# Kernel tuning notes

Measured on AMD Instinct MI355X. Metric: run time of the kernel, lower is better.

The kernel has to match this reference:

```python
import jax, jax.numpy as jnp
import numpy as np

B = 16384
IN = 512
H = 512

def setup_inputs() -> dict:
    key = jax.random.key(0)
    ks = jax.random.split(key, 8)
    inp = {
        "x_t": jax.random.normal(ks[0], (B, IN), dtype=jnp.float32),
        "h_t": jax.random.normal(ks[1], (B, H), dtype=jnp.float32),
        "W_ir": jax.random.normal(ks[2], (IN, H), dtype=jnp.float32),
        "W_hr": jax.random.normal(ks[3], (H, H), dtype=jnp.float32),
        "b_r": jnp.zeros((H,), dtype=jnp.float32),
        "W_iz": jax.random.normal(ks[4], (IN, H), dtype=jnp.float32),
        "W_hz": jax.random.normal(ks[5], (H, H), dtype=jnp.float32),
        "b_z": jnp.zeros((H,), dtype=jnp.float32),
        "W_in": jax.random.normal(ks[6], (IN, H), dtype=jnp.float32),
        "W_hn": jax.random.normal(ks[7], (H, H), dtype=jnp.float32),
        "b_n": jnp.zeros((H,), dtype=jnp.float32),
    }
    return inp

def reference(x_t, h_t, W_ir, W_hr, b_r, W_iz, W_hz, b_z, W_in, W_hn, b_n):
    # Fuse the three input-side and three hidden-side GEMMs by concatenating weights.
    Wi = jnp.concatenate([W_ir, W_iz, W_in], axis=1)   # [IN, 3H]
    Wh = jnp.concatenate([W_hr, W_hz, W_hn], axis=1)   # [H, 3H]
    gi = x_t @ Wi                                      # [B, 3H]
    gh = h_t @ Wh                                      # [B, 3H]
    h = b_r.shape[0]
    r_t = jax.nn.sigmoid(gi[:, :h] + gh[:, :h] + b_r)
    z_t = jax.nn.sigmoid(gi[:, h:2*h] + gh[:, h:2*h] + b_z)
    n_t = jnp.tanh(gi[:, 2*h:] + r_t * gh[:, 2*h:] + b_n)
    return (1.0 - z_t) * n_t + z_t * h_t
```

## Files before the change

kernel.cpp:

```cpp
#include <hip/hip_runtime.h>
#include <hip/hip_fp16.h>

typedef _Float16 half8 __attribute__((ext_vector_type(8)));
typedef float floatx4 __attribute__((ext_vector_type(4)));

#define AS1 __attribute__((address_space(1)))
#define AS3 __attribute__((address_space(3)))

#define WLO_OFF (6 * 512 * 512)

__device__ __forceinline__ void async_lds16(const void* g, void* l) {
  __builtin_amdgcn_global_load_lds((const AS1 void*)g, (AS3 void*)l, 16, 0, 0);
}

__global__ __launch_bounds__(256) void permute_w(
    const float* __restrict__ Wir, const float* __restrict__ Whr,
    const float* __restrict__ Wiz, const float* __restrict__ Whz,
    const float* __restrict__ Win, const float* __restrict__ Whn,
    _Float16* __restrict__ wperm) {
  __shared__ __align__(16) float tile[32 * 68];
  const int b = blockIdx.x;
  const int w = b >> 7;
  const int rem = b & 127;
  const int ki = rem >> 3;
  const int nt = rem & 7;
  const float* W = (w == 0) ? Wir : (w == 1) ? Whr : (w == 2) ? Wiz
                 : (w == 3) ? Whz : (w == 4) ? Win : Whn;
  const int k0 = ki * 32, n0 = nt * 64;
  const int t = threadIdx.x;

  const int kk = t >> 3;
  const int nn = (t & 7) * 8;
  const float* src = W + (k0 + kk) * 512 + n0 + nn;
  float4 f0 = *(const float4*)(src);
  float4 f1 = *(const float4*)(src + 4);
  float* drow = tile + kk * 68 + nn;
  *(float4*)(drow) = f0;
  *(float4*)(drow + 4) = f1;
  __syncthreads();

  const int u = t >> 6, l = t & 63;
  const int nloc = 16 * u + (l & 15);
  const int kbase = 8 * (l >> 4);
  half8 vh, vl;
#pragma unroll
  for (int j = 0; j < 8; ++j) {
    float f = tile[(kbase + j) * 68 + nloc];
    _Float16 hi = (_Float16)f;
    _Float16 lo = (_Float16)(f - (float)hi);
    vh[j] = hi;
    vl[j] = lo;
  }
  const size_t off = ((size_t)((w * 8 + nt) * 16 + ki)) * 2048 + t * 8;
  *(half8*)(wperm + off) = vh;
  *(half8*)(wperm + WLO_OFF + off) = vl;
}

__global__ __launch_bounds__(256, 2) void gru_fused(
    const float* __restrict__ x, const float* __restrict__ h,
    const _Float16* __restrict__ wperm,
    const float* __restrict__ br, const float* __restrict__ bz,
    const float* __restrict__ bn, float* __restrict__ out) {
  __shared__ __align__(16) _Float16 ldsXh[128 * 32];
  __shared__ __align__(16) _Float16 ldsXl[128 * 32];
  __shared__ __align__(16) _Float16 ldsHh[128 * 32];
  __shared__ __align__(16) _Float16 ldsHl[128 * 32];
  __shared__ __align__(16) _Float16 ldsW[6 * 2048];

  const int t = threadIdx.x;
  const int lane = t & 63;
  const int wv = t >> 6;
  const int wm = wv >> 1;
  const int wn = wv & 1;
  const int bid = blockIdx.x;
  const int nt = bid & 7;
  const int mt = bid >> 3;
  const int m0 = mt * 128;
  const int n0 = nt * 64;
  const _Float16* wlo = wperm + WLO_OFF;

  floatx4 acc_r[4][2] = {};
  floatx4 acc_z[4][2] = {};
  floatx4 acc_in[4][2] = {};
  floatx4 acc_hn[4][2] = {};

  const int c0 = t, c1 = t + 256;
  const int s0 = c0 >> 6, l0 = c0 & 63;
  const int s1 = c1 >> 6, l1 = c1 & 63;
  const int mA0 = 16 * s0 + (l0 & 15), kA0 = 8 * (l0 >> 4);
  const int mA1 = 16 * s1 + (l1 & 15), kA1 = 8 * (l1 >> 4);

  for (int kt = 0; kt < 16; ++kt) {
    const int k0 = kt * 32;
    __syncthreads();

#pragma unroll
    for (int q = 0; q < 6; ++q) {
      const int gg = wv * 6 + q;
      const int w = gg >> 2, u = gg & 3;
      const char* gsrc = (const char*)wperm +
          ((size_t)((w * 8 + nt) * 16 + kt)) * 4096 + u * 1024 + lane * 16;
      char* ldst = (char*)ldsW + (w * 4 + u) * 1024;
      async_lds16(gsrc, ldst);
    }

    {
      const float* px0 = x + (m0 + mA0) * 512 + k0 + kA0;
      const float* px1 = x + (m0 + mA1) * 512 + k0 + kA1;
      const float* ph0 = h + (m0 + mA0) * 512 + k0 + kA0;
      const float* ph1 = h + (m0 + mA1) * 512 + k0 + kA1;
      float v[4][8];
      *(float4*)&v[0][0] = *(const float4*)px0; *(float4*)&v[0][4] = *(const float4*)(px0 + 4);
      *(float4*)&v[1][0] = *(const float4*)px1; *(float4*)&v[1][4] = *(const float4*)(px1 + 4);
      *(float4*)&v[2][0] = *(const float4*)ph0; *(float4*)&v[2][4] = *(const float4*)(ph0 + 4);
      *(float4*)&v[3][0] = *(const float4*)ph1; *(float4*)&v[3][4] = *(const float4*)(ph1 + 4);
      half8 hi[4], lo[4];
#pragma unroll
      for (int g = 0; g < 4; ++g) {
#pragma unroll
        for (int j = 0; j < 8; ++j) {
          _Float16 a = (_Float16)v[g][j];
          hi[g][j] = a;
          lo[g][j] = (_Float16)(v[g][j] - (float)a);
        }
      }
      *(half8*)(ldsXh + c0 * 8) = hi[0]; *(half8*)(ldsXl + c0 * 8) = lo[0];
      *(half8*)(ldsXh + c1 * 8) = hi[1]; *(half8*)(ldsXl + c1 * 8) = lo[1];
      *(half8*)(ldsHh + c0 * 8) = hi[2]; *(half8*)(ldsHl + c0 * 8) = lo[2];
      *(half8*)(ldsHh + c1 * 8) = hi[3]; *(half8*)(ldsHl + c1 * 8) = lo[3];
    }
    __syncthreads();

    half8 axh[4], ahh[4];
#pragma unroll
    for (int i = 0; i < 4; ++i) {
      axh[i] = *(const half8*)(ldsXh + ((wm * 4 + i) * 64 + lane) * 8);
      ahh[i] = *(const half8*)(ldsHh + ((wm * 4 + i) * 64 + lane) * 8);
    }
#pragma unroll
    for (int jn = 0; jn < 2; ++jn) {
      const int bo = (wn * 2 + jn) * 512 + lane * 8;
      const size_t tb = ((size_t)(nt * 16 + kt)) * 2048 + bo;
      half8 bl_ir = *(const half8*)(wlo + tb + (size_t)0 * 8 * 16 * 2048);
      half8 bl_hr = *(const half8*)(wlo + tb + (size_t)1 * 8 * 16 * 2048);
      half8 bl_iz = *(const half8*)(wlo + tb + (size_t)2 * 8 * 16 * 2048);
      half8 bl_hz = *(const half8*)(wlo + tb + (size_t)3 * 8 * 16 * 2048);
      half8 bl_in = *(const half8*)(wlo + tb + (size_t)4 * 8 * 16 * 2048);
      half8 bl_hn = *(const half8*)(wlo + tb + (size_t)5 * 8 * 16 * 2048);
      half8 bh_ir = *(const half8*)(ldsW + 0 * 2048 + bo);
      half8 bh_hr = *(const half8*)(ldsW + 1 * 2048 + bo);
      half8 bh_iz = *(const half8*)(ldsW + 2 * 2048 + bo);
      half8 bh_hz = *(const half8*)(ldsW + 3 * 2048 + bo);
      half8 bh_in = *(const half8*)(ldsW + 4 * 2048 + bo);
      half8 bh_hn = *(const half8*)(ldsW + 5 * 2048 + bo);
#pragma unroll
      for (int i = 0; i < 4; ++i) {
        half8 axl = *(const half8*)(ldsXl + ((wm * 4 + i) * 64 + lane) * 8);
        half8 ahl = *(const half8*)(ldsHl + ((wm * 4 + i) * 64 + lane) * 8);
        acc_r[i][jn]  = __builtin_amdgcn_mfma_f32_16x16x32_f16(axh[i], bh_ir, acc_r[i][jn], 0, 0, 0);
        acc_r[i][jn]  = __builtin_amdgcn_mfma_f32_16x16x32_f16(axl,    bh_ir, acc_r[i][jn], 0, 0, 0);
        acc_r[i][jn]  = __builtin_amdgcn_mfma_f32_16x16x32_f16(ahh[i], bh_hr, acc_r[i][jn], 0, 0, 0);
        acc_r[i][jn]  = __builtin_amdgcn_mfma_f32_16x16x32_f16(ahl,    bh_hr, acc_r[i][jn], 0, 0, 0);
        acc_z[i][jn]  = __builtin_amdgcn_mfma_f32_16x16x32_f16(axh[i], bh_iz, acc_z[i][jn], 0, 0, 0);
        acc_z[i][jn]  = __builtin_amdgcn_mfma_f32_16x16x32_f16(axl,    bh_iz, acc_z[i][jn], 0, 0, 0);
        acc_z[i][jn]  = __builtin_amdgcn_mfma_f32_16x16x32_f16(ahh[i], bh_hz, acc_z[i][jn], 0, 0, 0);
        acc_z[i][jn]  = __builtin_amdgcn_mfma_f32_16x16x32_f16(ahl,    bh_hz, acc_z[i][jn], 0, 0, 0);
        acc_in[i][jn] = __builtin_amdgcn_mfma_f32_16x16x32_f16(axh[i], bh_in, acc_in[i][jn], 0, 0, 0);
        acc_in[i][jn] = __builtin_amdgcn_mfma_f32_16x16x32_f16(axl,    bh_in, acc_in[i][jn], 0, 0, 0);
        acc_hn[i][jn] = __builtin_amdgcn_mfma_f32_16x16x32_f16(ahh[i], bh_hn, acc_hn[i][jn], 0, 0, 0);
        acc_hn[i][jn] = __builtin_amdgcn_mfma_f32_16x16x32_f16(ahl,    bh_hn, acc_hn[i][jn], 0, 0, 0);
      }
#pragma unroll
      for (int i = 0; i < 4; ++i) {
        acc_r[i][jn]  = __builtin_amdgcn_mfma_f32_16x16x32_f16(axh[i], bl_ir, acc_r[i][jn], 0, 0, 0);
        acc_r[i][jn]  = __builtin_amdgcn_mfma_f32_16x16x32_f16(ahh[i], bl_hr, acc_r[i][jn], 0, 0, 0);
        acc_z[i][jn]  = __builtin_amdgcn_mfma_f32_16x16x32_f16(axh[i], bl_iz, acc_z[i][jn], 0, 0, 0);
        acc_z[i][jn]  = __builtin_amdgcn_mfma_f32_16x16x32_f16(ahh[i], bl_hz, acc_z[i][jn], 0, 0, 0);
        acc_in[i][jn] = __builtin_amdgcn_mfma_f32_16x16x32_f16(axh[i], bl_in, acc_in[i][jn], 0, 0, 0);
        acc_hn[i][jn] = __builtin_amdgcn_mfma_f32_16x16x32_f16(ahh[i], bl_hn, acc_hn[i][jn], 0, 0, 0);
      }
    }
  }

  const int quad = lane >> 4;
  const int col = lane & 15;
#pragma unroll
  for (int i = 0; i < 4; ++i) {
    const int mbase = m0 + wm * 64 + i * 16 + quad * 4;
#pragma unroll
    for (int jn = 0; jn < 2; ++jn) {
      const int n = n0 + wn * 32 + jn * 16 + col;
      const float vbr = br[n], vbz = bz[n], vbn = bn[n];
#pragma unroll
      for (int r = 0; r < 4; ++r) {
        const int m = mbase + r;
        const float gr = acc_r[i][jn][r] + vbr;
        const float gz = acc_z[i][jn][r] + vbz;
        const float rg = 1.0f / (1.0f + __expf(-gr));
        const float zg = 1.0f / (1.0f + __expf(-gz));
        const float gn = acc_in[i][jn][r] + rg * acc_hn[i][jn][r] + vbn;
        const float e2 = __expf(2.0f * gn);
        const float ntv = 1.0f - 2.0f / (e2 + 1.0f);
        const float hp = h[m * 512 + n];
        out[m * 512 + n] = (1.0f - zg) * ntv + zg * hp;
      }
    }
  }
}

extern "C" void kernel_launch(void* const* d_in, const int* in_sizes, int n_in,
                              void* d_out, int out_size, void* d_ws, size_t ws_size,
                              hipStream_t stream) {
  const float* x   = (const float*)d_in[0];
  const float* h   = (const float*)d_in[1];
  const float* Wir = (const float*)d_in[2];
  const float* Whr = (const float*)d_in[3];
  const float* br  = (const float*)d_in[4];
  const float* Wiz = (const float*)d_in[5];
  const float* Whz = (const float*)d_in[6];
  const float* bz  = (const float*)d_in[7];
  const float* Win = (const float*)d_in[8];
  const float* Whn = (const float*)d_in[9];
  const float* bn  = (const float*)d_in[10];
  float* out = (float*)d_out;
  _Float16* wperm = (_Float16*)d_ws;

  permute_w<<<768, 256, 0, stream>>>(Wir, Whr, Wiz, Whz, Win, Whn, wperm);
  gru_fused<<<1024, 256, 0, stream>>>(x, h, wperm, br, bz, bn, out);
}
```

Before: 282.2 us.

## Pre-split x/h into fp16 hi/lo tiles and stream them via async LDS loads

A preprocessing pass now converts x and h once into pre-tiled fp16 hi/lo buffers in the workspace. The main kernel then copies those tiles straight into LDS with global_load_lds, instead of loading fp32 and converting in registers on every block. Without this, each of the 8 N-tile blocks sharing an M-tile repeats the conversion. The change also adds an XCD-aware block swizzle so the blocks sharing an M-tile land on the same XCD. The cost is a large extra write and read of the converted activations through memory, and it needs a big workspace; if the workspace is too small, the code falls back to the old conversion path.

```diff
diff --git a/kernel.cpp b/kernel.cpp
--- a/kernel.cpp
+++ b/kernel.cpp
@@ -7,19 +7,55 @@
 #define AS1 __attribute__((address_space(1)))
 #define AS3 __attribute__((address_space(3)))
 
-#define WLO_OFF (6 * 512 * 512)
+#define WLO_OFF   (6 * 512 * 512)
+#define XH_BASE   (2 * WLO_OFF)
+#define XH_LO_OFF (2 * 16384 * 512)
+#define WS_NEED   ((size_t)(XH_BASE + 2 * XH_LO_OFF) * 2)
 
 __device__ __forceinline__ void async_lds16(const void* g, void* l) {
   __builtin_amdgcn_global_load_lds((const AS1 void*)g, (AS3 void*)l, 16, 0, 0);
 }
 
-__global__ __launch_bounds__(256) void permute_w(
+__global__ __launch_bounds__(256) void preprocess(
+    const float* __restrict__ x, const float* __restrict__ h,
     const float* __restrict__ Wir, const float* __restrict__ Whr,
     const float* __restrict__ Wiz, const float* __restrict__ Whz,
     const float* __restrict__ Win, const float* __restrict__ Whn,
-    _Float16* __restrict__ wperm) {
+    _Float16* __restrict__ ws, int do_xh) {
+  const int t = threadIdx.x;
+  const int bid = blockIdx.x;
+  if (do_xh && bid < 4096) {
+    const int mat = bid >> 11;
+    const int rem = bid & 2047;
+    const int mt = rem >> 4, kt = rem & 15;
+    const float* src = mat ? h : x;
+    const size_t tb = (size_t)(mat * 2048 + mt * 16 + kt) * 4096;
+    _Float16* hi = ws + XH_BASE;
+    _Float16* lo = hi + XH_LO_OFF;
+#pragma unroll
+    for (int cc = 0; cc < 2; ++cc) {
+      const int c = t + cc * 256;
+      const int l = c & 63, s = c >> 6;
+      const int m = mt * 128 + 16 * s + (l & 15);
+      const int k = kt * 32 + 8 * (l >> 4);
+      const float* p = src + (size_t)m * 512 + k;
+      float4 f0 = *(const float4*)p;
+      float4 f1 = *(const float4*)(p + 4);
+      float v[8] = {f0.x, f0.y, f0.z, f0.w, f1.x, f1.y, f1.z, f1.w};
+      half8 vh, vl;
+#pragma unroll
+      for (int j = 0; j < 8; ++j) {
+        _Float16 a = (_Float16)v[j];
+        vh[j] = a;
+        vl[j] = (_Float16)(v[j] - (float)a);
+      }
+      *(half8*)(hi + tb + c * 8) = vh;
+      *(half8*)(lo + tb + c * 8) = vl;
+    }
+    return;
+  }
+  const int b = do_xh ? (bid - 4096) : bid;
   __shared__ __align__(16) float tile[32 * 68];
-  const int b = blockIdx.x;
   const int w = b >> 7;
   const int rem = b & 127;
   const int ki = rem >> 3;
@@ -27,8 +63,6 @@
   const float* W = (w == 0) ? Wir : (w == 1) ? Whr : (w == 2) ? Wiz
                  : (w == 3) ? Whz : (w == 4) ? Win : Whn;
   const int k0 = ki * 32, n0 = nt * 64;
-  const int t = threadIdx.x;
-
   const int kk = t >> 3;
   const int nn = (t & 7) * 8;
   const float* src = W + (k0 + kk) * 512 + n0 + nn;
@@ -38,7 +72,6 @@
   *(float4*)(drow) = f0;
   *(float4*)(drow + 4) = f1;
   __syncthreads();
-
   const int u = t >> 6, l = t & 63;
   const int nloc = 16 * u + (l & 15);
   const int kbase = 8 * (l >> 4);
@@ -46,25 +79,30 @@
 #pragma unroll
   for (int j = 0; j < 8; ++j) {
     float f = tile[(kbase + j) * 68 + nloc];
-    _Float16 hi = (_Float16)f;
-    _Float16 lo = (_Float16)(f - (float)hi);
-    vh[j] = hi;
-    vl[j] = lo;
+    _Float16 hiv = (_Float16)f;
+    vh[j] = hiv;
+    vl[j] = (_Float16)(f - (float)hiv);
   }
   const size_t off = ((size_t)((w * 8 + nt) * 16 + ki)) * 2048 + t * 8;
-  *(half8*)(wperm + off) = vh;
-  *(half8*)(wperm + WLO_OFF + off) = vl;
-}
-
-__global__ __launch_bounds__(256, 2) void gru_fused(
-    const float* __restrict__ x, const float* __restrict__ h,
-    const _Float16* __restrict__ wperm,
+  *(half8*)(ws + off) = vh;
+  *(half8*)(ws + WLO_OFF + off) = vl;
+}
+
+__device__ __forceinline__ void swizzle_mn(int bid, int& mt, int& nt) {
+  const int xcd = bid & 7;
+  const int u = bid >> 3;
+  nt = u & 7;
+  mt = ((u >> 3) << 3) | xcd;
+}
+
+__global__ __launch_bounds__(256, 2) void gru_dma(
+    const float* __restrict__ h, const _Float16* __restrict__ ws,
     const float* __restrict__ br, const float* __restrict__ bz,
     const float* __restrict__ bn, float* __restrict__ out) {
-  __shared__ __align__(16) _Float16 ldsXh[128 * 32];
-  __shared__ __align__(16) _Float16 ldsXl[128 * 32];
-  __shared__ __align__(16) _Float16 ldsHh[128 * 32];
-  __shared__ __align__(16) _Float16 ldsHl[128 * 32];
+  __shared__ __align__(16) _Float16 ldsXh[4096];
+  __shared__ __align__(16) _Float16 ldsXl[4096];
+  __shared__ __align__(16) _Float16 ldsHh[4096];
+  __shared__ __align__(16) _Float16 ldsHl[4096];
   __shared__ __align__(16) _Float16 ldsW[6 * 2048];
 
   const int t = threadIdx.x;
@@ -72,62 +110,47 @@
   const int wv = t >> 6;
   const int wm = wv >> 1;
   const int wn = wv & 1;
-  const int bid = blockIdx.x;
-  const int nt = bid & 7;
-  const int mt = bid >> 3;
+  int mt, nt;
+  swizzle_mn(blockIdx.x, mt, nt);
   const int m0 = mt * 128;
   const int n0 = nt * 64;
-  const _Float16* wlo = wperm + WLO_OFF;
+
+  const _Float16* whi = ws;
+  const _Float16* wlo = ws + WLO_OFF;
+  const _Float16* xhhi = ws + XH_BASE;
+  const _Float16* xhlo = xhhi + XH_LO_OFF;
 
   floatx4 acc_r[4][2] = {};
   floatx4 acc_z[4][2] = {};
   floatx4 acc_in[4][2] = {};
   floatx4 acc_hn[4][2] = {};
 
-  const int c0 = t, c1 = t + 256;
-  const int s0 = c0 >> 6, l0 = c0 & 63;
-  const int s1 = c1 >> 6, l1 = c1 & 63;
-  const int mA0 = 16 * s0 + (l0 & 15), kA0 = 8 * (l0 >> 4);
-  const int mA1 = 16 * s1 + (l1 & 15), kA1 = 8 * (l1 >> 4);
-
   for (int kt = 0; kt < 16; ++kt) {
-    const int k0 = kt * 32;
     __syncthreads();
 
 #pragma unroll
-    for (int q = 0; q < 6; ++q) {
-      const int gg = wv * 6 + q;
-      const int w = gg >> 2, u = gg & 3;
-      const char* gsrc = (const char*)wperm +
-          ((size_t)((w * 8 + nt) * 16 + kt)) * 4096 + u * 1024 + lane * 16;
-      char* ldst = (char*)ldsW + (w * 4 + u) * 1024;
+    for (int q = 0; q < 14; ++q) {
+      const int g = wv * 14 + q;
+      const char* gsrc;
+      char* ldst;
+      if (g < 24) {
+        const int w = g >> 2, uu = g & 3;
+        gsrc = (const char*)whi + ((size_t)((w * 8 + nt) * 16 + kt)) * 4096 +
+               uu * 1024 + (size_t)lane * 16;
+        ldst = (char*)ldsW + (w * 4 + uu) * 1024;
+      } else {
+        const int g2 = g - 24;
+        const int buf = g2 >> 3, seg = g2 & 7;
+        const int mat = buf >> 1;
+        const int part = buf & 1;
+        const _Float16* base = part ? xhlo : xhhi;
+        gsrc = (const char*)base + ((size_t)(mat * 2048 + mt * 16 + kt)) * 8192 +
+               seg * 1024 + (size_t)lane * 16;
+        _Float16* lb = (buf == 0) ? ldsXh : (buf == 1) ? ldsXl
+                     : (buf == 2) ? ldsHh : ldsHl;
+        ldst = (char*)lb + seg * 1024;
+      }
       async_lds16(gsrc, ldst);
-    }
-
-    {
-      const float* px0 = x + (m0 + mA0) * 512 + k0 + kA0;
-      const float* px1 = x + (m0 + mA1) * 512 + k0 + kA1;
-      const float* ph0 = h + (m0 + mA0) * 512 + k0 + kA0;
-      const float* ph1 = h + (m0 + mA1) * 512 + k0 + kA1;
-      float v[4][8];
-      *(float4*)&v[0][0] = *(const float4*)px0; *(float4*)&v[0][4] = *(const float4*)(px0 + 4);
-      *(float4*)&v[1][0] = *(const float4*)px1; *(float4*)&v[1][4] = *(const float4*)(px1 + 4);
-      *(float4*)&v[2][0] = *(const float4*)ph0; *(float4*)&v[2][4] = *(const float4*)(ph0 + 4);
-      *(float4*)&v[3][0] = *(const float4*)ph1; *(float4*)&v[3][4] = *(const float4*)(ph1 + 4);
-      half8 hi[4], lo[4];
-#pragma unroll
-      for (int g = 0; g < 4; ++g) {
-#pragma unroll
-        for (int j = 0; j < 8; ++j) {
-          _Float16 a = (_Float16)v[g][j];
-          hi[g][j] = a;
-          lo[g][j] = (_Float16)(v[g][j] - (float)a);
-        }
-      }
-      *(half8*)(ldsXh + c0 * 8) = hi[0]; *(half8*)(ldsXl + c0 * 8) = lo[0];
-      *(half8*)(ldsXh + c1 * 8) = hi[1]; *(half8*)(ldsXl + c1 * 8) = lo[1];
-      *(half8*)(ldsHh + c0 * 8) = hi[2]; *(half8*)(ldsHl + c0 * 8) = lo[2];
-      *(half8*)(ldsHh + c1 * 8) = hi[3]; *(half8*)(ldsHl + c1 * 8) = lo[3];
     }
     __syncthreads();
 
@@ -208,6 +231,155 @@
   }
 }
 
+__global__ __launch_bounds__(256, 2) void gru_conv(
+    const float* __restrict__ x, const float* __restrict__ h,
+    const _Float16* __restrict__ wperm,
+    const float* __restrict__ br, const float* __restrict__ bz,
+    const float* __restrict__ bn, float* __restrict__ out) {
+  __shared__ __align__(16) _Float16 ldsXh[128 * 32];
+  __shared__ __align__(16) _Float16 ldsXl[128 * 32];
+  __shared__ __align__(16) _Float16 ldsHh[128 * 32];
+  __shared__ __align__(16) _Float16 ldsHl[128 * 32];
+  __shared__ __align__(16) _Float16 ldsW[6 * 2048];
+
+  const int t = threadIdx.x;
+  const int lane = t & 63;
+  const int wv = t >> 6;
+  const int wm = wv >> 1;
+  const int wn = wv & 1;
+  int mt, nt;
+  swizzle_mn(blockIdx.x, mt, nt);
+  const int m0 = mt * 128;
+  const int n0 = nt * 64;
+  const _Float16* wlo = wperm + WLO_OFF;
+
+  floatx4 acc_r[4][2] = {};
+  floatx4 acc_z[4][2] = {};
+  floatx4 acc_in[4][2] = {};
+  floatx4 acc_hn[4][2] = {};
+
+  const int c0 = t, c1 = t + 256;
+  const int s0 = c0 >> 6, l0 = c0 & 63;
+  const int s1 = c1 >> 6, l1 = c1 & 63;
+  const int mA0 = 16 * s0 + (l0 & 15), kA0 = 8 * (l0 >> 4);
+  const int mA1 = 16 * s1 + (l1 & 15), kA1 = 8 * (l1 >> 4);
+
+  for (int kt = 0; kt < 16; ++kt) {
+    const int k0 = kt * 32;
+    __syncthreads();
+#pragma unroll
+    for (int q = 0; q < 6; ++q) {
+      const int gg = wv * 6 + q;
+      const int w = gg >> 2, u = gg & 3;
+      const char* gsrc = (const char*)wperm +
+          ((size_t)((w * 8 + nt) * 16 + kt)) * 4096 + u * 1024 + lane * 16;
+      char* ldst = (char*)ldsW + (w * 4 + u) * 1024;
+      async_lds16(gsrc, ldst);
+    }
+    {
+      const float* px0 = x + (m0 + mA0) * 512 + k0 + kA0;
+      const float* px1 = x + (m0 + mA1) * 512 + k0 + kA1;
+      const float* ph0 = h + (m0 + mA0) * 512 + k0 + kA0;
+      const float* ph1 = h + (m0 + mA1) * 512 + k0 + kA1;
+      float v[4][8];
+      *(float4*)&v[0][0] = *(const float4*)px0; *(float4*)&v[0][4] = *(const float4*)(px0 + 4);
+      *(float4*)&v[1][0] = *(const float4*)px1; *(float4*)&v[1][4] = *(const float4*)(px1 + 4);
+      *(float4*)&v[2][0] = *(const float4*)ph0; *(float4*)&v[2][4] = *(const float4*)(ph0 + 4);
+      *(float4*)&v[3][0] = *(const float4*)ph1; *(float4*)&v[3][4] = *(const float4*)(ph1 + 4);
+      half8 hi[4], lo[4];
+#pragma unroll
+      for (int g = 0; g < 4; ++g) {
+#pragma unroll
+        for (int j = 0; j < 8; ++j) {
+          _Float16 a = (_Float16)v[g][j];
+          hi[g][j] = a;
+          lo[g][j] = (_Float16)(v[g][j] - (float)a);
+        }
+      }
+      *(half8*)(ldsXh + c0 * 8) = hi[0]; *(half8*)(ldsXl + c0 * 8) = lo[0];
+      *(half8*)(ldsXh + c1 * 8) = hi[1]; *(half8*)(ldsXl + c1 * 8) = lo[1];
+      *(half8*)(ldsHh + c0 * 8) = hi[2]; *(half8*)(ldsHl + c0 * 8) = lo[2];
+      *(half8*)(ldsHh + c1 * 8) = hi[3]; *(half8*)(ldsHl + c1 * 8) = lo[3];
+    }
+    __syncthreads();
+
+    half8 axh[4], ahh[4];
+#pragma unroll
+    for (int i = 0; i < 4; ++i) {
+      axh[i] = *(const half8*)(ldsXh + ((wm * 4 + i) * 64 + lane) * 8);
+      ahh[i] = *(const half8*)(ldsHh + ((wm * 4 + i) * 64 + lane) * 8);
+    }
+#pragma unroll
+    for (int jn = 0; jn < 2; ++jn) {
+      const int bo = (wn * 2 + jn) * 512 + lane * 8;
+      const size_t tb = ((size_t)(nt * 16 + kt)) * 2048 + bo;
+      half8 bl_ir = *(const half8*)(wlo + tb + (size_t)0 * 8 * 16 * 2048);
+      half8 bl_hr = *(const half8*)(wlo + tb + (size_t)1 * 8 * 16 * 2048);
+      half8 bl_iz = *(const half8*)(wlo + tb + (size_t)2 * 8 * 16 * 2048);
+      half8 bl_hz = *(const half8*)(wlo + tb + (size_t)3 * 8 * 16 * 2048);
+      half8 bl_in = *(const half8*)(wlo + tb + (size_t)4 * 8 * 16 * 2048);
+      half8 bl_hn = *(const half8*)(wlo + tb + (size_t)5 * 8 * 16 * 2048);
+      half8 bh_ir = *(const half8*)(ldsW + 0 * 2048 + bo);
+      half8 bh_hr = *(const half8*)(ldsW + 1 * 2048 + bo);
+      half8 bh_iz = *(const half8*)(ldsW + 2 * 2048 + bo);
+      half8 bh_hz = *(const half8*)(ldsW + 3 * 2048 + bo);
+      half8 bh_in = *(const half8*)(ldsW + 4 * 2048 + bo);
+      half8 bh_hn = *(const half8*)(ldsW + 5 * 2048 + bo);
+#pragma unroll
+      for (int i = 0; i < 4; ++i) {
+        half8 axl = *(const half8*)(ldsXl + ((wm * 4 + i) * 64 + lane) * 8);
+        half8 ahl = *(const half8*)(ldsHl + ((wm * 4 + i) * 64 + lane) * 8);
+        acc_r[i][jn]  = __builtin_amdgcn_mfma_f32_16x16x32_f16(axh[i], bh_ir, acc_r[i][jn], 0, 0, 0);
+        acc_r[i][jn]  = __builtin_amdgcn_mfma_f32_16x16x32_f16(axl,    bh_ir, acc_r[i][jn], 0, 0, 0);
+        acc_r[i][jn]  = __builtin_amdgcn_mfma_f32_16x16x32_f16(ahh[i], bh_hr, acc_r[i][jn], 0, 0, 0);
+        acc_r[i][jn]  = __builtin_amdgcn_mfma_f32_16x16x32_f16(ahl,    bh_hr, acc_r[i][jn], 0, 0, 0);
+        acc_z[i][jn]  = __builtin_amdgcn_mfma_f32_16x16x32_f16(axh[i], bh_iz, acc_z[i][jn], 0, 0, 0);
+        acc_z[i][jn]  = __builtin_amdgcn_mfma_f32_16x16x32_f16(axl,    bh_iz, acc_z[i][jn], 0, 0, 0);
+        acc_z[i][jn]  = __builtin_amdgcn_mfma_f32_16x16x32_f16(ahh[i], bh_hz, acc_z[i][jn], 0, 0, 0);
+        acc_z[i][jn]  = __builtin_amdgcn_mfma_f32_16x16x32_f16(ahl,    bh_hz, acc_z[i][jn], 0, 0, 0);
+        acc_in[i][jn] = __builtin_amdgcn_mfma_f32_16x16x32_f16(axh[i], bh_in, acc_in[i][jn], 0, 0, 0);
+        acc_in[i][jn] = __builtin_amdgcn_mfma_f32_16x16x32_f16(axl,    bh_in, acc_in[i][jn], 0, 0, 0);
+        acc_hn[i][jn] = __builtin_amdgcn_mfma_f32_16x16x32_f16(ahh[i], bh_hn, acc_hn[i][jn], 0, 0, 0);
+        acc_hn[i][jn] = __builtin_amdgcn_mfma_f32_16x16x32_f16(ahl,    bh_hn, acc_hn[i][jn], 0, 0, 0);
+      }
+#pragma unroll
+      for (int i = 0; i < 4; ++i) {
+        acc_r[i][jn]  = __builtin_amdgcn_mfma_f32_16x16x32_f16(axh[i], bl_ir, acc_r[i][jn], 0, 0, 0);
+        acc_r[i][jn]  = __builtin_amdgcn_mfma_f32_16x16x32_f16(ahh[i], bl_hr, acc_r[i][jn], 0, 0, 0);
+        acc_z[i][jn]  = __builtin_amdgcn_mfma_f32_16x16x32_f16(axh[i], bl_iz, acc_z[i][jn], 0, 0, 0);
+        acc_z[i][jn]  = __builtin_amdgcn_mfma_f32_16x16x32_f16(ahh[i], bl_hz, acc_z[i][jn], 0, 0, 0);
+        acc_in[i][jn] = __builtin_amdgcn_mfma_f32_16x16x32_f16(axh[i], bl_in, acc_in[i][jn], 0, 0, 0);
+        acc_hn[i][jn] = __builtin_amdgcn_mfma_f32_16x16x32_f16(ahh[i], bl_hn, acc_hn[i][jn], 0, 0, 0);
+      }
+    }
+  }
+
+  const int quad = lane >> 4;
+  const int col = lane & 15;
+#pragma unroll
+  for (int i = 0; i < 4; ++i) {
+    const int mbase = m0 + wm * 64 + i * 16 + quad * 4;
+#pragma unroll
+    for (int jn = 0; jn < 2; ++jn) {
+      const int n = n0 + wn * 32 + jn * 16 + col;
+      const float vbr = br[n], vbz = bz[n], vbn = bn[n];
+#pragma unroll
+      for (int r = 0; r < 4; ++r) {
+        const int m = mbase + r;
+        const float gr = acc_r[i][jn][r] + vbr;
+        const float gz = acc_z[i][jn][r] + vbz;
+        const float rg = 1.0f / (1.0f + __expf(-gr));
+        const float zg = 1.0f / (1.0f + __expf(-gz));
+        const float gn = acc_in[i][jn][r] + rg * acc_hn[i][jn][r] + vbn;
+        const float e2 = __expf(2.0f * gn);
+        const float ntv = 1.0f - 2.0f / (e2 + 1.0f);
+        const float hp = h[m * 512 + n];
+        out[m * 512 + n] = (1.0f - zg) * ntv + zg * hp;
+      }
+    }
+  }
+}
+
 extern "C" void kernel_launch(void* const* d_in, const int* in_sizes, int n_in,
                               void* d_out, int out_size, void* d_ws, size_t ws_size,
                               hipStream_t stream) {
@@ -223,8 +395,13 @@
   const float* Whn = (const float*)d_in[9];
   const float* bn  = (const float*)d_in[10];
   float* out = (float*)d_out;
-  _Float16* wperm = (_Float16*)d_ws;
-
-  permute_w<<<768, 256, 0, stream>>>(Wir, Whr, Wiz, Whz, Win, Whn, wperm);
-  gru_fused<<<1024, 256, 0, stream>>>(x, h, wperm, br, bz, bn, out);
-}
+  _Float16* ws = (_Float16*)d_ws;
+
+  if (ws_size >= WS_NEED) {
+    preprocess<<<4096 + 768, 256, 0, stream>>>(x, h, Wir, Whr, Wiz, Whz, Win, Whn, ws, 1);
+    gru_dma<<<1024, 256, 0, stream>>>(h, ws, br, bz, bn, out);
+  } else {
+    preprocess<<<768, 256, 0, stream>>>(x, h, Wir, Whr, Wiz, Whz, Win, Whn, ws, 0);
+    gru_conv<<<1024, 256, 0, stream>>>(x, h, ws, br, bz, bn, out);
+  }
+}
```

Measured after the change: 500.7 us. +77.4%, slower.

## Prefetch next x/h tile into registers and read hi weights directly from global

Applied to the files above, without the earlier changes.

Register-prefetches the next K-slice of x and h during the MFMA loop and converts it to hi/lo fp16 after the compute, so global load latency overlaps with math. It also drops the async global-to-LDS staging of the high-part weights and loads them straight from global/L2 into registers, as the low parts already were. This cuts LDS usage and a sync dependency but adds register pressure and more uncoalesced-free global weight reads per wave. The final iteration prefetches a wrapped slice that is never used.

```diff
diff --git a/kernel.cpp b/kernel.cpp
--- a/kernel.cpp
+++ b/kernel.cpp
@@ -4,14 +4,8 @@
 typedef _Float16 half8 __attribute__((ext_vector_type(8)));
 typedef float floatx4 __attribute__((ext_vector_type(4)));
 
-#define AS1 __attribute__((address_space(1)))
-#define AS3 __attribute__((address_space(3)))
-
 #define WLO_OFF (6 * 512 * 512)
-
-__device__ __forceinline__ void async_lds16(const void* g, void* l) {
-  __builtin_amdgcn_global_load_lds((const AS1 void*)g, (AS3 void*)l, 16, 0, 0);
-}
+#define WSTRIDE ((size_t)(8 * 16 * 2048))
 
 __global__ __launch_bounds__(256) void permute_w(
     const float* __restrict__ Wir, const float* __restrict__ Whr,
@@ -46,14 +40,24 @@
 #pragma unroll
   for (int j = 0; j < 8; ++j) {
     float f = tile[(kbase + j) * 68 + nloc];
-    _Float16 hi = (_Float16)f;
-    _Float16 lo = (_Float16)(f - (float)hi);
-    vh[j] = hi;
-    vl[j] = lo;
+    _Float16 hiv = (_Float16)f;
+    vh[j] = hiv;
+    vl[j] = (_Float16)(f - (float)hiv);
   }
   const size_t off = ((size_t)((w * 8 + nt) * 16 + ki)) * 2048 + t * 8;
   *(half8*)(wperm + off) = vh;
   *(half8*)(wperm + WLO_OFF + off) = vl;
+}
+
+__device__ __forceinline__ void cvt_hilo(const float4 a, const float4 b,
+                                         half8& hi, half8& lo) {
+  const float v[8] = {a.x, a.y, a.z, a.w, b.x, b.y, b.z, b.w};
+#pragma unroll
+  for (int j = 0; j < 8; ++j) {
+    _Float16 hv = (_Float16)v[j];
+    hi[j] = hv;
+    lo[j] = (_Float16)(v[j] - (float)hv);
+  }
 }
 
 __global__ __launch_bounds__(256, 2) void gru_fused(
@@ -61,11 +65,10 @@
     const _Float16* __restrict__ wperm,
     const float* __restrict__ br, const float* __restrict__ bz,
     const float* __restrict__ bn, float* __restrict__ out) {
-  __shared__ __align__(16) _Float16 ldsXh[128 * 32];
-  __shared__ __align__(16) _Float16 ldsXl[128 * 32];
-  __shared__ __align__(16) _Float16 ldsHh[128 * 32];
-  __shared__ __align__(16) _Float16 ldsHl[128 * 32];
-  __shared__ __align__(16) _Float16 ldsW[6 * 2048];
+  __shared__ __align__(16) _Float16 ldsXh[4096];
+  __shared__ __align__(16) _Float16 ldsXl[4096];
+  __shared__ __align__(16) _Float16 ldsHh[4096];
+  __shared__ __align__(16) _Float16 ldsHl[4096];
 
   const int t = threadIdx.x;
   const int lane = t & 63;
@@ -77,6 +80,7 @@
   const int mt = bid >> 3;
   const int m0 = mt * 128;
   const int n0 = nt * 64;
+  const _Float16* whi = wperm;
   const _Float16* wlo = wperm + WLO_OFF;
 
   floatx4 acc_r[4][2] = {};
@@ -85,51 +89,41 @@
   floatx4 acc_hn[4][2] = {};
 
   const int c0 = t, c1 = t + 256;
-  const int s0 = c0 >> 6, l0 = c0 & 63;
-  const int s1 = c1 >> 6, l1 = c1 & 63;
-  const int mA0 = 16 * s0 + (l0 & 15), kA0 = 8 * (l0 >> 4);
-  const int mA1 = 16 * s1 + (l1 & 15), kA1 = 8 * (l1 >> 4);
+  const int l0 = c0 & 63, l1 = c1 & 63;
+  const int mA0 = 16 * (c0 >> 6) + (l0 & 15), kA0 = 8 * (l0 >> 4);
+  const int mA1 = 16 * (c1 >> 6) + (l1 & 15), kA1 = 8 * (l1 >> 4);
+  const float* pxb0 = x + (size_t)(m0 + mA0) * 512 + kA0;
+  const float* pxb1 = x + (size_t)(m0 + mA1) * 512 + kA1;
+  const float* phb0 = h + (size_t)(m0 + mA0) * 512 + kA0;
+  const float* phb1 = h + (size_t)(m0 + mA1) * 512 + kA1;
+
+  half8 sth[4], stl[4];
+  cvt_hilo(*(const float4*)pxb0, *(const float4*)(pxb0 + 4), sth[0], stl[0]);
+  cvt_hilo(*(const float4*)pxb1, *(const float4*)(pxb1 + 4), sth[1], stl[1]);
+  cvt_hilo(*(const float4*)phb0, *(const float4*)(phb0 + 4), sth[2], stl[2]);
+  cvt_hilo(*(const float4*)phb1, *(const float4*)(phb1 + 4), sth[3], stl[3]);
 
   for (int kt = 0; kt < 16; ++kt) {
-    const int k0 = kt * 32;
     __syncthreads();
-
-#pragma unroll
-    for (int q = 0; q < 6; ++q) {
-      const int gg = wv * 6 + q;
-      const int w = gg >> 2, u = gg & 3;
-      const char* gsrc = (const char*)wperm +
-          ((size_t)((w * 8 + nt) * 16 + kt)) * 4096 + u * 1024 + lane * 16;
-      char* ldst = (char*)ldsW + (w * 4 + u) * 1024;
-      async_lds16(gsrc, ldst);
-    }
-
-    {
-      const float* px0 = x + (m0 + mA0) * 512 + k0 + kA0;
-      const float* px1 = x + (m0 + mA1) * 512 + k0 + kA1;
-      const float* ph0 = h + (m0 + mA0) * 512 + k0 + kA0;
-      const float* ph1 = h + (m0 + mA1) * 512 + k0 + kA1;
-      float v[4][8];
-      *(float4*)&v[0][0] = *(const float4*)px0; *(float4*)&v[0][4] = *(const float4*)(px0 + 4);
-      *(float4*)&v[1][0] = *(const float4*)px1; *(float4*)&v[1][4] = *(const float4*)(px1 + 4);
-      *(float4*)&v[2][0] = *(const float4*)ph0; *(float4*)&v[2][4] = *(const float4*)(ph0 + 4);
-      *(float4*)&v[3][0] = *(const float4*)ph1; *(float4*)&v[3][4] = *(const float4*)(ph1 + 4);
-      half8 hi[4], lo[4];
-#pragma unroll
-      for (int g = 0; g < 4; ++g) {
-#pragma unroll
-        for (int j = 0; j < 8; ++j) {
-          _Float16 a = (_Float16)v[g][j];
-          hi[g][j] = a;
-          lo[g][j] = (_Float16)(v[g][j] - (float)a);
-        }
-      }
-      *(half8*)(ldsXh + c0 * 8) = hi[0]; *(half8*)(ldsXl + c0 * 8) = lo[0];
-      *(half8*)(ldsXh + c1 * 8) = hi[1]; *(half8*)(ldsXl + c1 * 8) = lo[1];
-      *(half8*)(ldsHh + c0 * 8) = hi[2]; *(half8*)(ldsHl + c0 * 8) = lo[2];
-      *(half8*)(ldsHh + c1 * 8) = hi[3]; *(half8*)(ldsHl + c1 * 8) = lo[3];
-    }
+    *(half8*)(ldsXh + c0 * 8) = sth[0];
+    *(half8*)(ldsXh + c1 * 8) = sth[1];
+    *(half8*)(ldsHh + c0 * 8) = sth[2];
+    *(half8*)(ldsHh + c1 * 8) = sth[3];
+    *(half8*)(ldsXl + c0 * 8) = stl[0];
+    *(half8*)(ldsXl + c1 * 8) = stl[1];
+    *(half8*)(ldsHl + c0 * 8) = stl[2];
+    *(half8*)(ldsHl + c1 * 8) = stl[3];
     __syncthreads();
+
+    const int kn = ((kt + 1) & 15) * 32;
+    float4 nx0 = *(const float4*)(pxb0 + kn);
+    float4 nx1 = *(const float4*)(pxb0 + kn + 4);
+    float4 nx2 = *(const float4*)(pxb1 + kn);
+    float4 nx3 = *(const float4*)(pxb1 + kn + 4);
+    float4 nh0 = *(const float4*)(phb0 + kn);
+    float4 nh1 = *(const float4*)(phb0 + kn + 4);
+    float4 nh2 = *(const float4*)(phb1 + kn);
+    float4 nh3 = *(const float4*)(phb1 + kn + 4);
 
     half8 axh[4], ahh[4];
 #pragma unroll
@@ -141,18 +135,12 @@
     for (int jn = 0; jn < 2; ++jn) {
       const int bo = (wn * 2 + jn) * 512 + lane * 8;
       const size_t tb = ((size_t)(nt * 16 + kt)) * 2048 + bo;
-      half8 bl_ir = *(const half8*)(wlo + tb + (size_t)0 * 8 * 16 * 2048);
-      half8 bl_hr = *(const half8*)(wlo + tb + (size_t)1 * 8 * 16 * 2048);
-      half8 bl_iz = *(const half8*)(wlo + tb + (size_t)2 * 8 * 16 * 2048);
-      half8 bl_hz = *(const half8*)(wlo + tb + (size_t)3 * 8 * 16 * 2048);
-      half8 bl_in = *(const half8*)(wlo + tb + (size_t)4 * 8 * 16 * 2048);
-      half8 bl_hn = *(const half8*)(wlo + tb + (size_t)5 * 8 * 16 * 2048);
-      half8 bh_ir = *(const half8*)(ldsW + 0 * 2048 + bo);
-      half8 bh_hr = *(const half8*)(ldsW + 1 * 2048 + bo);
-      half8 bh_iz = *(const half8*)(ldsW + 2 * 2048 + bo);
-      half8 bh_hz = *(const half8*)(ldsW + 3 * 2048 + bo);
-      half8 bh_in = *(const half8*)(ldsW + 4 * 2048 + bo);
-      half8 bh_hn = *(const half8*)(ldsW + 5 * 2048 + bo);
+      half8 bh_ir = *(const half8*)(whi + tb + 0 * WSTRIDE);
+      half8 bh_hr = *(const half8*)(whi + tb + 1 * WSTRIDE);
+      half8 bh_iz = *(const half8*)(whi + tb + 2 * WSTRIDE);
+      half8 bh_hz = *(const half8*)(whi + tb + 3 * WSTRIDE);
+      half8 bh_in = *(const half8*)(whi + tb + 4 * WSTRIDE);
+      half8 bh_hn = *(const half8*)(whi + tb + 5 * WSTRIDE);
 #pragma unroll
       for (int i = 0; i < 4; ++i) {
         half8 axl = *(const half8*)(ldsXl + ((wm * 4 + i) * 64 + lane) * 8);
@@ -170,6 +158,12 @@
         acc_hn[i][jn] = __builtin_amdgcn_mfma_f32_16x16x32_f16(ahh[i], bh_hn, acc_hn[i][jn], 0, 0, 0);
         acc_hn[i][jn] = __builtin_amdgcn_mfma_f32_16x16x32_f16(ahl,    bh_hn, acc_hn[i][jn], 0, 0, 0);
       }
+      half8 bl_ir = *(const half8*)(wlo + tb + 0 * WSTRIDE);
+      half8 bl_hr = *(const half8*)(wlo + tb + 1 * WSTRIDE);
+      half8 bl_iz = *(const half8*)(wlo + tb + 2 * WSTRIDE);
+      half8 bl_hz = *(const half8*)(wlo + tb + 3 * WSTRIDE);
+      half8 bl_in = *(const half8*)(wlo + tb + 4 * WSTRIDE);
+      half8 bl_hn = *(const half8*)(wlo + tb + 5 * WSTRIDE);
 #pragma unroll
       for (int i = 0; i < 4; ++i) {
         acc_r[i][jn]  = __builtin_amdgcn_mfma_f32_16x16x32_f16(axh[i], bl_ir, acc_r[i][jn], 0, 0, 0);
@@ -180,6 +174,11 @@
         acc_hn[i][jn] = __builtin_amdgcn_mfma_f32_16x16x32_f16(ahh[i], bl_hn, acc_hn[i][jn], 0, 0, 0);
       }
     }
+
+    cvt_hilo(nx0, nx1, sth[0], stl[0]);
+    cvt_hilo(nx2, nx3, sth[1], stl[1]);
+    cvt_hilo(nh0, nh1, sth[2], stl[2]);
+    cvt_hilo(nh2, nh3, sth[3], stl[3]);
   }
 
   const int quad = lane >> 4;
@@ -201,8 +200,8 @@
         const float gn = acc_in[i][jn][r] + rg * acc_hn[i][jn][r] + vbn;
         const float e2 = __expf(2.0f * gn);
         const float ntv = 1.0f - 2.0f / (e2 + 1.0f);
-        const float hp = h[m * 512 + n];
-        out[m * 512 + n] = (1.0f - zg) * ntv + zg * hp;
+        const float hp = h[(size_t)m * 512 + n];
+        out[(size_t)m * 512 + n] = (1.0f - zg) * ntv + zg * hp;
       }
     }
   }
```

Result: no change. 286.2 us (+1.4%).
